# Optimization experiments

Hardware: AMD Instinct MI355X
Metric: run time of the kernel (lower is better)

## Reference

```python
import jax, jax.numpy as jnp
import numpy as np

K, STRIDE, PAD, DIL = 3, 1, 1, 1
EPS = 1e-20


def kernel_channels(x):
    # x: [B, C, H, W] -> [B, C, K*K, H', W'] (row-major kernel ordering, as torch F.unfold)
    xp = jnp.pad(x, ((0, 0), (0, 0), (PAD, PAD), (PAD, PAD)))
    Hp, Wp = xp.shape[2], xp.shape[3]
    Ho = (Hp - DIL * (K - 1) - 1) // STRIDE + 1
    Wo = (Wp - DIL * (K - 1) - 1) // STRIDE + 1
    patches = [xp[:, :, i * DIL:i * DIL + (Ho - 1) * STRIDE + 1:STRIDE,
                       j * DIL:j * DIL + (Wo - 1) * STRIDE + 1:STRIDE]
               for i in range(K) for j in range(K)]
    return jnp.stack(patches, axis=2)


def setup_inputs() -> dict:
    key = jax.random.key(0)
    ks = jax.random.split(key, 8)
    B, Cin, Cout, H, W = 4, 32, 32, 256, 256
    d = jax.random.normal(ks[0], (B, Cin, H, W), jnp.float32)
    cd = jax.random.uniform(ks[1], (B, Cin, H, W), jnp.float32)          # confidences in [0,1)
    s = jax.random.uniform(ks[2], (B, Cin, H, W), jnp.float32)           # unused in forward (API compat)
    cs = jax.random.uniform(ks[3], (B, Cin, H, W), jnp.float32)          # unused in forward (API compat)
    s_prod_roll = jax.random.uniform(ks[4], (B, Cin, K * K, H, W), jnp.float32)
    channel_weight = jax.random.normal(ks[5], (Cout, Cin, 1, 1), jnp.float32)
    spatial_weight = jax.random.normal(ks[6], (Cin, 1, K * K, 1, 1), jnp.float32)
    bias = jax.random.normal(ks[7], (1, Cout, 1, 1), jnp.float32) * 0.01
    return {"d": d, "cd": cd, "s": s, "cs": cs, "s_prod_roll": s_prod_roll,
            "channel_weight": channel_weight, "spatial_weight": spatial_weight, "bias": bias}


def reference(d, cd, s, cs, s_prod_roll, channel_weight, spatial_weight, bias):
    # EnforcePos: weights are passed through softplus before use
    sw = jax.nn.softplus(spatial_weight)[:, 0, :, 0, 0]   # [Cin, K*K]
    cw = jax.nn.softplus(channel_weight)[:, :, 0, 0]      # [Cout, Cin]

    d_roll = kernel_channels(d)                            # [B, Cin, K*K, H, W]
    cd_roll = kernel_channels(cd)
    cd_prop = cd_roll * s_prod_roll

    # conv3d with groups=Cin, depth kernel K*K == per-channel weighted sum over neighbor axis
    nom = jnp.einsum('bckhw,ck->bchw', cd_prop * d_roll, sw)
    denom = jnp.einsum('bckhw,ck->bchw', cd_prop, sw)
    d_spatial = nom / (denom + EPS)
    cd_spatial = denom / jnp.sum(sw)

    # 1x1 conv2d, groups=1 == channel mixing
    nom2 = jnp.einsum('bchw,oc->bohw', cd_spatial * d_spatial, cw)
    denom2 = jnp.einsum('bchw,oc->bohw', cd_spatial, cw)
    d_out = nom2 / (denom2 + EPS) + bias
    cd_out = denom2 / jnp.sum(cw) / (STRIDE * STRIDE)
    return d_out, cd_out
```

## Files before the change

### kernel.cpp

```cpp
#include <hip/hip_runtime.h>

#define EPS 1e-20f
typedef float f4 __attribute__((ext_vector_type(4)));

__global__ void prep_weights(const float* __restrict__ channel_weight,
                             const float* __restrict__ spatial_weight,
                             float* __restrict__ ws) {
    __shared__ float red[256];
    int tid = threadIdx.x;
    float local_sw = 0.f, local_cw = 0.f;
    for (int i = tid; i < 288; i += 256) {
        float x = spatial_weight[i];
        float v = fmaxf(x, 0.f) + log1pf(expf(-fabsf(x)));
        ws[i] = v;
        local_sw += v;
    }
    for (int i = tid; i < 1024; i += 256) {
        float x = channel_weight[i];
        float v = fmaxf(x, 0.f) + log1pf(expf(-fabsf(x)));
        int o = i >> 5, c = i & 31;
        ws[288 + c * 32 + o] = v;
        local_cw += v;
    }
    red[tid] = local_sw;
    __syncthreads();
    for (int s = 128; s > 0; s >>= 1) {
        if (tid < s) red[tid] += red[tid + s];
        __syncthreads();
    }
    if (tid == 0) ws[1312] = 1.0f / red[0];
    __syncthreads();
    red[tid] = local_cw;
    __syncthreads();
    for (int s = 128; s > 0; s >>= 1) {
        if (tid < s) red[tid] += red[tid + s];
        __syncthreads();
    }
    if (tid == 0) ws[1313] = 1.0f / red[0];
}

__global__ __launch_bounds__(256) void fused6(
    const float* __restrict__ d,
    const float* __restrict__ cd,
    const float* __restrict__ sp,
    const float* __restrict__ wsbuf,
    const float* __restrict__ bias,
    float* __restrict__ out)
{
    __shared__ float lt[32 * 128];
    __shared__ float lc[32 * 128];
    __shared__ float lcw[1024];

    const int plane = 65536;

    int bid = blockIdx.x;
    bid = (bid & 7) * 256 + (bid >> 3);

    const int ct = bid & 1;
    const int h  = (bid >> 1) & 255;
    const int b  = bid >> 9;

    const int tid = threadIdx.x;

    #pragma unroll
    for (int i = 0; i < 4; ++i) lcw[i * 256 + tid] = wsbuf[288 + i * 256 + tid];

    const int w    = tid >> 6;
    const int half = (tid >> 5) & 1;
    const int pq   = tid & 31;
    const int col0 = ct * 128 + pq * 4;
    const float inv_sum_sw = wsbuf[1312];
    const bool rowv0 = (h >= 1), rowv2 = (h <= 254);

    #pragma unroll 1
    for (int iter = 0; iter < 4; ++iter) {
        const int c  = w * 8 + iter * 2 + half;
        const int bc = b * 32 + c;
        const float* __restrict__ dC  = d  + (size_t)bc * plane;
        const float* __restrict__ cdC = cd + (size_t)bc * plane;
        const float* __restrict__ spC = sp + (size_t)bc * 9 * plane + h * 256;

        f4 spv[9];
        #pragma unroll
        for (int k = 0; k < 9; ++k)
            spv[k] = __builtin_nontemporal_load((const f4*)(spC + (size_t)k * plane + col0));

        float dr[3][6], cr[3][6];
        #pragma unroll
        for (int i = 0; i < 3; ++i) {
            const int hh = h + i - 1;
            const int hc = min(max(hh, 0), 255);
            const float* __restrict__ drow = dC  + hc * 256;
            const float* __restrict__ crow = cdC + hc * 256;
            f4 dv = *(const f4*)(drow + col0);
            f4 cv = *(const f4*)(crow + col0);
            dr[i][1] = dv[0]; dr[i][2] = dv[1]; dr[i][3] = dv[2]; dr[i][4] = dv[3];
            cr[i][1] = cv[0]; cr[i][2] = cv[1]; cr[i][3] = cv[2]; cr[i][4] = cv[3];
            dr[i][0] = drow[max(col0 - 1, 0)];
            cr[i][0] = crow[max(col0 - 1, 0)];
            dr[i][5] = drow[min(col0 + 4, 255)];
            cr[i][5] = crow[min(col0 + 4, 255)];
        }

        float swk[9];
        #pragma unroll
        for (int k = 0; k < 9; ++k) swk[k] = wsbuf[c * 9 + k];

        float nom[4] = {0.f, 0.f, 0.f, 0.f}, den[4] = {0.f, 0.f, 0.f, 0.f};
        #pragma unroll
        for (int i = 0; i < 3; ++i) {
            const bool rv = (i == 0) ? rowv0 : ((i == 2) ? rowv2 : true);
            #pragma unroll
            for (int j = 0; j < 3; ++j) {
                const int k = i * 3 + j;
                const float s = swk[k];
                #pragma unroll
                for (int p = 0; p < 4; ++p) {
                    const int ww = col0 + p + j - 1;
                    const bool valid = rv && ((unsigned)ww < 256u);
                    const float cdp = valid ? cr[i][p + j] * spv[k][p] : 0.f;
                    nom[p] = fmaf(cdp * dr[i][p + j], s, nom[p]);
                    den[p] = fmaf(cdp, s, den[p]);
                }
            }
        }

        f4 tv, cv4;
        #pragma unroll
        for (int p = 0; p < 4; ++p) {
            tv[p]  = nom[p] * inv_sum_sw;
            cv4[p] = den[p] * inv_sum_sw;
        }
        *(f4*)&lt[c * 128 + pq * 4] = tv;
        *(f4*)&lc[c * 128 + pq * 4] = cv4;
    }

    __syncthreads();

    const int og = tid >> 5;
    const int o0 = og * 4;

    float n2[4][4], d2[4][4];
    #pragma unroll
    for (int oi = 0; oi < 4; ++oi)
        #pragma unroll
        for (int j = 0; j < 4; ++j) { n2[oi][j] = 0.f; d2[oi][j] = 0.f; }

    for (int cc = 0; cc < 32; ++cc) {
        const f4 tq = *(const f4*)&lt[cc * 128 + pq * 4];
        const f4 cq = *(const f4*)&lc[cc * 128 + pq * 4];
        const f4 cw4 = *(const f4*)&lcw[cc * 32 + o0];
        #pragma unroll
        for (int oi = 0; oi < 4; ++oi)
            #pragma unroll
            for (int j = 0; j < 4; ++j) {
                n2[oi][j] = fmaf(tq[j], cw4[oi], n2[oi][j]);
                d2[oi][j] = fmaf(cq[j], cw4[oi], d2[oi][j]);
            }
    }

    const float inv_sum_cw = wsbuf[1313];
    const f4 b4 = *(const f4*)&bias[o0];
    const int colb = ct * 128 + pq * 4;

    #pragma unroll
    for (int oi = 0; oi < 4; ++oi) {
        f4 dv, cv;
        #pragma unroll
        for (int j = 0; j < 4; ++j) {
            dv[j] = n2[oi][j] / (d2[oi][j] + EPS) + b4[oi];
            cv[j] = d2[oi][j] * inv_sum_cw;
        }
        const size_t po = (size_t)(b * 32 + o0 + oi) * plane + h * 256 + colb;
        *(f4*)(out + po)           = dv;
        *(f4*)(out + 8388608 + po) = cv;
    }
}

extern "C" void kernel_launch(void* const* d_in, const int* in_sizes, int n_in,
                              void* d_out, int out_size, void* d_ws, size_t ws_size,
                              hipStream_t stream) {
    const float* d    = (const float*)d_in[0];
    const float* cd   = (const float*)d_in[1];
    const float* sp   = (const float*)d_in[4];
    const float* cwt  = (const float*)d_in[5];
    const float* swt  = (const float*)d_in[6];
    const float* bias = (const float*)d_in[7];
    float* out = (float*)d_out;
    float* ws  = (float*)d_ws;

    prep_weights<<<1, 256, 0, stream>>>(cwt, swt, ws);
    fused6<<<2048, 256, 0, stream>>>(d, cd, sp, ws, bias, out);
}
```

Before: 94.97 us.

## Shrink column tile to 64 and double block count with occupancy hint

Each block now covers a 64-column quarter row instead of a 128-column half row, so twice as many blocks launch. The channel-mixing stage gives each thread two output channels instead of four, and shared-memory tiles shrink by half. A launch-bounds hint asking for 8 waves per SIMD is added to lower register use and raise occupancy for this memory-bound kernel. In exchange, halo columns are reloaded more often, the channel weights are loaded into shared memory per block twice as many times in total, and reads per thread are shorter.

```diff
diff --git a/kernel.cpp b/kernel.cpp
--- a/kernel.cpp
+++ b/kernel.cpp
@@ -39,7 +39,7 @@
     if (tid == 0) ws[1313] = 1.0f / red[0];
 }
 
-__global__ __launch_bounds__(256) void fused6(
+__global__ __launch_bounds__(256, 8) void fused7(
     const float* __restrict__ d,
     const float* __restrict__ cd,
     const float* __restrict__ sp,
@@ -47,18 +47,18 @@
     const float* __restrict__ bias,
     float* __restrict__ out)
 {
-    __shared__ float lt[32 * 128];
-    __shared__ float lc[32 * 128];
+    __shared__ float lt[32 * 64];
+    __shared__ float lc[32 * 64];
     __shared__ float lcw[1024];
 
     const int plane = 65536;
 
     int bid = blockIdx.x;
-    bid = (bid & 7) * 256 + (bid >> 3);
+    bid = (bid & 7) * 512 + (bid >> 3);
 
-    const int ct = bid & 1;
-    const int h  = (bid >> 1) & 255;
-    const int b  = bid >> 9;
+    const int qt = bid & 3;
+    const int h  = (bid >> 2) & 255;
+    const int b  = bid >> 10;
 
     const int tid = threadIdx.x;
 
@@ -66,15 +66,15 @@
     for (int i = 0; i < 4; ++i) lcw[i * 256 + tid] = wsbuf[288 + i * 256 + tid];
 
     const int w    = tid >> 6;
-    const int half = (tid >> 5) & 1;
-    const int pq   = tid & 31;
-    const int col0 = ct * 128 + pq * 4;
+    const int cs   = (tid >> 4) & 3;
+    const int pq   = tid & 15;
+    const int col0 = qt * 64 + pq * 4;
     const float inv_sum_sw = wsbuf[1312];
     const bool rowv0 = (h >= 1), rowv2 = (h <= 254);
 
     #pragma unroll 1
-    for (int iter = 0; iter < 4; ++iter) {
-        const int c  = w * 8 + iter * 2 + half;
+    for (int iter = 0; iter < 2; ++iter) {
+        const int c  = w * 8 + iter * 4 + cs;
         const int bc = b * 32 + c;
         const float* __restrict__ dC  = d  + (size_t)bc * plane;
         const float* __restrict__ cdC = cd + (size_t)bc * plane;
@@ -131,47 +131,47 @@
             tv[p]  = nom[p] * inv_sum_sw;
             cv4[p] = den[p] * inv_sum_sw;
         }
-        *(f4*)&lt[c * 128 + pq * 4] = tv;
-        *(f4*)&lc[c * 128 + pq * 4] = cv4;
+        *(f4*)&lt[c * 64 + pq * 4] = tv;
+        *(f4*)&lc[c * 64 + pq * 4] = cv4;
     }
 
     __syncthreads();
 
-    const int og = tid >> 5;
-    const int o0 = og * 4;
+    const int og = tid >> 4;
+    const int o0 = og * 2;
 
-    float n2[4][4], d2[4][4];
+    float n2[2][4], d2[2][4];
     #pragma unroll
-    for (int oi = 0; oi < 4; ++oi)
+    for (int oi = 0; oi < 2; ++oi)
         #pragma unroll
         for (int j = 0; j < 4; ++j) { n2[oi][j] = 0.f; d2[oi][j] = 0.f; }
 
     for (int cc = 0; cc < 32; ++cc) {
-        const f4 tq = *(const f4*)&lt[cc * 128 + pq * 4];
-        const f4 cq = *(const f4*)&lc[cc * 128 + pq * 4];
-        const f4 cw4 = *(const f4*)&lcw[cc * 32 + o0];
+        const f4 tq = *(const f4*)&lt[cc * 64 + pq * 4];
+        const f4 cq = *(const f4*)&lc[cc * 64 + pq * 4];
+        const float cw0 = lcw[cc * 32 + o0];
+        const float cw1 = lcw[cc * 32 + o0 + 1];
         #pragma unroll
-        for (int oi = 0; oi < 4; ++oi)
-            #pragma unroll
-            for (int j = 0; j < 4; ++j) {
-                n2[oi][j] = fmaf(tq[j], cw4[oi], n2[oi][j]);
-                d2[oi][j] = fmaf(cq[j], cw4[oi], d2[oi][j]);
-            }
+        for (int j = 0; j < 4; ++j) {
+            n2[0][j] = fmaf(tq[j], cw0, n2[0][j]);
+            d2[0][j] = fmaf(cq[j], cw0, d2[0][j]);
+            n2[1][j] = fmaf(tq[j], cw1, n2[1][j]);
+            d2[1][j] = fmaf(cq[j], cw1, d2[1][j]);
+        }
     }
 
     const float inv_sum_cw = wsbuf[1313];
-    const f4 b4 = *(const f4*)&bias[o0];
-    const int colb = ct * 128 + pq * 4;
 
     #pragma unroll
-    for (int oi = 0; oi < 4; ++oi) {
+    for (int oi = 0; oi < 2; ++oi) {
+        const float bo = bias[o0 + oi];
         f4 dv, cv;
         #pragma unroll
         for (int j = 0; j < 4; ++j) {
-            dv[j] = n2[oi][j] / (d2[oi][j] + EPS) + b4[oi];
+            dv[j] = n2[oi][j] / (d2[oi][j] + EPS) + bo;
             cv[j] = d2[oi][j] * inv_sum_cw;
         }
-        const size_t po = (size_t)(b * 32 + o0 + oi) * plane + h * 256 + colb;
+        const size_t po = (size_t)(b * 32 + o0 + oi) * plane + h * 256 + col0;
         *(f4*)(out + po)           = dv;
         *(f4*)(out + 8388608 + po) = cv;
     }
@@ -190,5 +190,5 @@
     float* ws  = (float*)d_ws;
 
     prep_weights<<<1, 256, 0, stream>>>(cwt, swt, ws);
-    fused6<<<2048, 256, 0, stream>>>(d, cd, sp, ws, bias, out);
+    fused7<<<4096, 256, 0, stream>>>(d, cd, sp, ws, bias, out);
 }
```

Measured after the change: 305.3 us. +221.5%, slower.

## Process both column tiles per block and prefetch second tile during channel mix

Applied to the files above, without the earlier changes.

Each block now handles a full 256-wide row (two 128-column tiles) instead of one, halving the grid. The first channel's loads for the second tile are issued before the first tile's channel-mixing stage, so global memory latency can overlap with LDS/FMA work. This adds register pressure for the extra prefetched tile and one more barrier. It also reduces the number of resident blocks available to hide latency.

```diff
diff --git a/kernel.cpp b/kernel.cpp
--- a/kernel.cpp
+++ b/kernel.cpp
@@ -39,7 +39,128 @@
     if (tid == 0) ws[1313] = 1.0f / red[0];
 }
 
-__global__ __launch_bounds__(256) void fused6(
+struct TileRegs {
+    f4 spv[9];
+    f4 dv[3], cv[3];
+    float dl[3], cl[3], dh[3], ch[3];
+};
+
+__device__ __forceinline__ void tile_load(TileRegs& T,
+        const float* __restrict__ d, const float* __restrict__ cd,
+        const float* __restrict__ sp, int bc, int h, int col0) {
+    const int plane = 65536;
+    const float* __restrict__ dC  = d  + (size_t)bc * plane;
+    const float* __restrict__ cdC = cd + (size_t)bc * plane;
+    const float* __restrict__ spC = sp + (size_t)bc * 9 * plane + h * 256;
+    #pragma unroll
+    for (int k = 0; k < 9; ++k)
+        T.spv[k] = __builtin_nontemporal_load((const f4*)(spC + (size_t)k * plane + col0));
+    #pragma unroll
+    for (int i = 0; i < 3; ++i) {
+        const int hc = min(max(h + i - 1, 0), 255);
+        const float* __restrict__ drow = dC  + hc * 256;
+        const float* __restrict__ crow = cdC + hc * 256;
+        T.dv[i] = *(const f4*)(drow + col0);
+        T.cv[i] = *(const f4*)(crow + col0);
+        T.dl[i] = drow[max(col0 - 1, 0)];
+        T.cl[i] = crow[max(col0 - 1, 0)];
+        T.dh[i] = drow[min(col0 + 4, 255)];
+        T.ch[i] = crow[min(col0 + 4, 255)];
+    }
+}
+
+__device__ __forceinline__ void tile_compute_store(const TileRegs& T,
+        float* __restrict__ lt, float* __restrict__ lc,
+        const float* __restrict__ wsbuf, int c, int col0, int pq,
+        float inv_sum_sw, bool rowv0, bool rowv2) {
+    float dr[3][6], cr[3][6];
+    #pragma unroll
+    for (int i = 0; i < 3; ++i) {
+        dr[i][0] = T.dl[i]; cr[i][0] = T.cl[i];
+        #pragma unroll
+        for (int p = 0; p < 4; ++p) { dr[i][p + 1] = T.dv[i][p]; cr[i][p + 1] = T.cv[i][p]; }
+        dr[i][5] = T.dh[i]; cr[i][5] = T.ch[i];
+    }
+    float swk[9];
+    #pragma unroll
+    for (int k = 0; k < 9; ++k) swk[k] = wsbuf[c * 9 + k];
+
+    float nom[4] = {0.f, 0.f, 0.f, 0.f}, den[4] = {0.f, 0.f, 0.f, 0.f};
+    #pragma unroll
+    for (int i = 0; i < 3; ++i) {
+        const bool rv = (i == 0) ? rowv0 : ((i == 2) ? rowv2 : true);
+        #pragma unroll
+        for (int j = 0; j < 3; ++j) {
+            const int k = i * 3 + j;
+            const float s = swk[k];
+            #pragma unroll
+            for (int p = 0; p < 4; ++p) {
+                const int ww = col0 + p + j - 1;
+                const bool valid = rv && ((unsigned)ww < 256u);
+                const float cdp = valid ? cr[i][p + j] * T.spv[k][p] : 0.f;
+                nom[p] = fmaf(cdp * dr[i][p + j], s, nom[p]);
+                den[p] = fmaf(cdp, s, den[p]);
+            }
+        }
+    }
+    f4 tv, cv4;
+    #pragma unroll
+    for (int p = 0; p < 4; ++p) {
+        tv[p]  = nom[p] * inv_sum_sw;
+        cv4[p] = den[p] * inv_sum_sw;
+    }
+    *(f4*)&lt[c * 128 + pq * 4] = tv;
+    *(f4*)&lc[c * 128 + pq * 4] = cv4;
+}
+
+__device__ __forceinline__ void stage2_emit(
+        const float* __restrict__ lt, const float* __restrict__ lc,
+        const float* __restrict__ lcw, const float* __restrict__ wsbuf,
+        const float* __restrict__ bias, float* __restrict__ out,
+        int b, int h, int ct, int tid) {
+    const int plane = 65536;
+    const int og = tid >> 5;
+    const int pq = tid & 31;
+    const int o0 = og * 4;
+
+    float n2[4][4], d2[4][4];
+    #pragma unroll
+    for (int oi = 0; oi < 4; ++oi)
+        #pragma unroll
+        for (int j = 0; j < 4; ++j) { n2[oi][j] = 0.f; d2[oi][j] = 0.f; }
+
+    for (int cc = 0; cc < 32; ++cc) {
+        const f4 tq = *(const f4*)&lt[cc * 128 + pq * 4];
+        const f4 cq = *(const f4*)&lc[cc * 128 + pq * 4];
+        const f4 cw4 = *(const f4*)&lcw[cc * 32 + o0];
+        #pragma unroll
+        for (int oi = 0; oi < 4; ++oi)
+            #pragma unroll
+            for (int j = 0; j < 4; ++j) {
+                n2[oi][j] = fmaf(tq[j], cw4[oi], n2[oi][j]);
+                d2[oi][j] = fmaf(cq[j], cw4[oi], d2[oi][j]);
+            }
+    }
+
+    const float inv_sum_cw = wsbuf[1313];
+    const f4 b4 = *(const f4*)&bias[o0];
+    const int colb = ct * 128 + pq * 4;
+
+    #pragma unroll
+    for (int oi = 0; oi < 4; ++oi) {
+        f4 dv, cv;
+        #pragma unroll
+        for (int j = 0; j < 4; ++j) {
+            dv[j] = n2[oi][j] / (d2[oi][j] + EPS) + b4[oi];
+            cv[j] = d2[oi][j] * inv_sum_cw;
+        }
+        const size_t po = (size_t)(b * 32 + o0 + oi) * plane + h * 256 + colb;
+        *(f4*)(out + po)           = dv;
+        *(f4*)(out + 8388608 + po) = cv;
+    }
+}
+
+__global__ __launch_bounds__(256) void fused9(
     const float* __restrict__ d,
     const float* __restrict__ cd,
     const float* __restrict__ sp,
@@ -51,14 +172,11 @@
     __shared__ float lc[32 * 128];
     __shared__ float lcw[1024];
 
-    const int plane = 65536;
-
     int bid = blockIdx.x;
-    bid = (bid & 7) * 256 + (bid >> 3);
-
-    const int ct = bid & 1;
-    const int h  = (bid >> 1) & 255;
-    const int b  = bid >> 9;
+    bid = (bid & 7) * 128 + (bid >> 3);
+
+    const int h = bid & 255;
+    const int b = bid >> 8;
 
     const int tid = threadIdx.x;
 
@@ -68,113 +186,42 @@
     const int w    = tid >> 6;
     const int half = (tid >> 5) & 1;
     const int pq   = tid & 31;
-    const int col0 = ct * 128 + pq * 4;
+    const int colT0 = pq * 4;
+    const int colT1 = 128 + pq * 4;
     const float inv_sum_sw = wsbuf[1312];
     const bool rowv0 = (h >= 1), rowv2 = (h <= 254);
 
+    TileRegs T, P;
+
     #pragma unroll 1
     for (int iter = 0; iter < 4; ++iter) {
-        const int c  = w * 8 + iter * 2 + half;
-        const int bc = b * 32 + c;
-        const float* __restrict__ dC  = d  + (size_t)bc * plane;
-        const float* __restrict__ cdC = cd + (size_t)bc * plane;
-        const float* __restrict__ spC = sp + (size_t)bc * 9 * plane + h * 256;
-
-        f4 spv[9];
-        #pragma unroll
-        for (int k = 0; k < 9; ++k)
-            spv[k] = __builtin_nontemporal_load((const f4*)(spC + (size_t)k * plane + col0));
-
-        float dr[3][6], cr[3][6];
-        #pragma unroll
-        for (int i = 0; i < 3; ++i) {
-            const int hh = h + i - 1;
-            const int hc = min(max(hh, 0), 255);
-            const float* __restrict__ drow = dC  + hc * 256;
-            const float* __restrict__ crow = cdC + hc * 256;
-            f4 dv = *(const f4*)(drow + col0);
-            f4 cv = *(const f4*)(crow + col0);
-            dr[i][1] = dv[0]; dr[i][2] = dv[1]; dr[i][3] = dv[2]; dr[i][4] = dv[3];
-            cr[i][1] = cv[0]; cr[i][2] = cv[1]; cr[i][3] = cv[2]; cr[i][4] = cv[3];
-            dr[i][0] = drow[max(col0 - 1, 0)];
-            cr[i][0] = crow[max(col0 - 1, 0)];
-            dr[i][5] = drow[min(col0 + 4, 255)];
-            cr[i][5] = crow[min(col0 + 4, 255)];
-        }
-
-        float swk[9];
-        #pragma unroll
-        for (int k = 0; k < 9; ++k) swk[k] = wsbuf[c * 9 + k];
-
-        float nom[4] = {0.f, 0.f, 0.f, 0.f}, den[4] = {0.f, 0.f, 0.f, 0.f};
-        #pragma unroll
-        for (int i = 0; i < 3; ++i) {
-            const bool rv = (i == 0) ? rowv0 : ((i == 2) ? rowv2 : true);
-            #pragma unroll
-            for (int j = 0; j < 3; ++j) {
-                const int k = i * 3 + j;
-                const float s = swk[k];
-                #pragma unroll
-                for (int p = 0; p < 4; ++p) {
-                    const int ww = col0 + p + j - 1;
-                    const bool valid = rv && ((unsigned)ww < 256u);
-                    const float cdp = valid ? cr[i][p + j] * spv[k][p] : 0.f;
-                    nom[p] = fmaf(cdp * dr[i][p + j], s, nom[p]);
-                    den[p] = fmaf(cdp, s, den[p]);
-                }
-            }
-        }
-
-        f4 tv, cv4;
-        #pragma unroll
-        for (int p = 0; p < 4; ++p) {
-            tv[p]  = nom[p] * inv_sum_sw;
-            cv4[p] = den[p] * inv_sum_sw;
-        }
-        *(f4*)&lt[c * 128 + pq * 4] = tv;
-        *(f4*)&lc[c * 128 + pq * 4] = cv4;
-    }
-
-    __syncthreads();
-
-    const int og = tid >> 5;
-    const int o0 = og * 4;
-
-    float n2[4][4], d2[4][4];
-    #pragma unroll
-    for (int oi = 0; oi < 4; ++oi)
-        #pragma unroll
-        for (int j = 0; j < 4; ++j) { n2[oi][j] = 0.f; d2[oi][j] = 0.f; }
-
-    for (int cc = 0; cc < 32; ++cc) {
-        const f4 tq = *(const f4*)&lt[cc * 128 + pq * 4];
-        const f4 cq = *(const f4*)&lc[cc * 128 + pq * 4];
-        const f4 cw4 = *(const f4*)&lcw[cc * 32 + o0];
-        #pragma unroll
-        for (int oi = 0; oi < 4; ++oi)
-            #pragma unroll
-            for (int j = 0; j < 4; ++j) {
-                n2[oi][j] = fmaf(tq[j], cw4[oi], n2[oi][j]);
-                d2[oi][j] = fmaf(cq[j], cw4[oi], d2[oi][j]);
-            }
-    }
-
-    const float inv_sum_cw = wsbuf[1313];
-    const f4 b4 = *(const f4*)&bias[o0];
-    const int colb = ct * 128 + pq * 4;
-
-    #pragma unroll
-    for (int oi = 0; oi < 4; ++oi) {
-        f4 dv, cv;
-        #pragma unroll
-        for (int j = 0; j < 4; ++j) {
-            dv[j] = n2[oi][j] / (d2[oi][j] + EPS) + b4[oi];
-            cv[j] = d2[oi][j] * inv_sum_cw;
-        }
-        const size_t po = (size_t)(b * 32 + o0 + oi) * plane + h * 256 + colb;
-        *(f4*)(out + po)           = dv;
-        *(f4*)(out + 8388608 + po) = cv;
-    }
+        const int c = w * 8 + iter * 2 + half;
+        tile_load(T, d, cd, sp, b * 32 + c, h, colT0);
+        tile_compute_store(T, lt, lc, wsbuf, c, colT0, pq, inv_sum_sw, rowv0, rowv2);
+    }
+    __syncthreads();
+
+    {
+        const int c0 = w * 8 + half;
+        tile_load(P, d, cd, sp, b * 32 + c0, h, colT1);
+    }
+
+    stage2_emit(lt, lc, lcw, wsbuf, bias, out, b, h, 0, tid);
+    __syncthreads();
+
+    {
+        const int c0 = w * 8 + half;
+        tile_compute_store(P, lt, lc, wsbuf, c0, colT1, pq, inv_sum_sw, rowv0, rowv2);
+    }
+    #pragma unroll 1
+    for (int iter = 1; iter < 4; ++iter) {
+        const int c = w * 8 + iter * 2 + half;
+        tile_load(T, d, cd, sp, b * 32 + c, h, colT1);
+        tile_compute_store(T, lt, lc, wsbuf, c, colT1, pq, inv_sum_sw, rowv0, rowv2);
+    }
+    __syncthreads();
+
+    stage2_emit(lt, lc, lcw, wsbuf, bias, out, b, h, 1, tid);
 }
 
 extern "C" void kernel_launch(void* const* d_in, const int* in_sizes, int n_in,
@@ -190,5 +237,5 @@
     float* ws  = (float*)d_ws;
 
     prep_weights<<<1, 256, 0, stream>>>(cwt, swt, ws);
-    fused6<<<2048, 256, 0, stream>>>(d, cd, sp, ws, bias, out);
-}
+    fused9<<<1024, 256, 0, stream>>>(d, cd, sp, ws, bias, out);
+}
```

Result: slower. 97.75 us (+2.9%).
